# Performance work log

Measured on AMD Instinct MI355X. Metric: run time of the kernel, lower is better.

Reference implementation:

```python
import jax, jax.numpy as jnp
import numpy as np
from jax import lax

B, C_IN, H, W = 16, 2048, 16, 16
HIDDEN, N_ANC = 512, 9
N_POS, N_NEG = 2048, 2048
TOT = B * N_ANC * H * W  # 36864 = flat conf logits; also rows of reg.view(-1,4)


def _xyxy_to_cxcywh(b):
    x1, y1, x2, y2 = b[..., 0], b[..., 1], b[..., 2], b[..., 3]
    return jnp.stack([(x1 + x2) * 0.5, (y1 + y2) * 0.5, x2 - x1, y2 - y1], axis=-1)


def _cxcywh_to_xyxy(b):
    cx, cy, w, h = b[..., 0], b[..., 1], b[..., 2], b[..., 3]
    return jnp.stack([cx - w * 0.5, cy - h * 0.5, cx + w * 0.5, cy + h * 0.5], axis=-1)


def _rand_boxes(key, n):
    # valid xyxy boxes on the 16x16 feature-map coordinate grid, w,h in [1,4]
    k1, k2 = jax.random.split(key)
    xy = jax.random.uniform(k1, (n, 2), jnp.float32) * 12.0
    wh = 1.0 + jax.random.uniform(k2, (n, 2), jnp.float32) * 3.0
    return jnp.concatenate([xy, xy + wh], axis=-1)


def setup_inputs() -> dict:
    key = jax.random.key(0)
    ks = jax.random.split(key, 10)
    feature_map = jax.random.normal(ks[0], (B, C_IN, H, W), jnp.float32)
    pos_anc_ind = jax.random.randint(ks[1], (N_POS,), 0, TOT)
    neg_anc_ind = jax.random.randint(ks[2], (N_NEG,), 0, TOT)
    pos_anc_coords = _rand_boxes(ks[3], N_POS)
    gt_bboxes_pos = _rand_boxes(ks[4], N_POS)
    s1 = 1.0 / np.sqrt(C_IN * 9)
    W1 = jax.random.uniform(ks[5], (HIDDEN, C_IN, 3, 3), jnp.float32, -s1, s1)
    b1 = jnp.zeros((HIDDEN,), jnp.float32)
    s2 = 1.0 / np.sqrt(HIDDEN)
    Wc = jax.random.uniform(ks[6], (N_ANC, HIDDEN), jnp.float32, -s2, s2)
    bc = jnp.zeros((N_ANC,), jnp.float32)
    Wr = jax.random.uniform(ks[7], (N_ANC * 4, HIDDEN), jnp.float32, -s2, s2)
    br = jnp.zeros((N_ANC * 4,), jnp.float32)
    return {"feature_map": feature_map, "pos_anc_coords": pos_anc_coords,
            "gt_bboxes_pos": gt_bboxes_pos, "W1": W1, "b1": b1, "Wc": Wc,
            "bc": bc, "Wr": Wr, "br": br,
            "pos_anc_ind": pos_anc_ind, "neg_anc_ind": neg_anc_ind}


def generate_proposals(anchors, offsets):
    a = _xyxy_to_cxcywh(anchors)
    p = jnp.stack([a[:, 0] + offsets[:, 0] * a[:, 2],
                   a[:, 1] + offsets[:, 1] * a[:, 3],
                   a[:, 2] * jnp.exp(offsets[:, 2]),
                   a[:, 3] * jnp.exp(offsets[:, 3])], axis=-1)
    return _cxcywh_to_xyxy(p)


def calc_gt_offsets(anc, gt):
    a = _xyxy_to_cxcywh(anc)
    g = _xyxy_to_cxcywh(gt)
    tx = (g[:, 0] - a[:, 0]) / a[:, 2]
    ty = (g[:, 1] - a[:, 1]) / a[:, 3]
    tw = jnp.log(g[:, 2] / a[:, 2])
    th = jnp.log(g[:, 3] / a[:, 3])
    return jnp.stack([tx, ty, tw, th], axis=-1)


def reference(feature_map, pos_anc_coords, gt_bboxes_pos, W1, b1, Wc, bc, Wr, br,
              pos_anc_ind, neg_anc_ind):
    # ProposalModule: conv3x3 -> (dropout=identity in eval) -> relu -> 1x1 heads
    out = lax.conv_general_dilated(feature_map, W1, (1, 1), 'SAME',
                                   dimension_numbers=('NCHW', 'OIHW', 'NCHW'))
    out = jax.nn.relu(out + b1[None, :, None, None])
    conf = jnp.einsum('bchw,oc->bohw', out, Wc) + bc[None, :, None, None]   # [B,9,H,W]
    reg = jnp.einsum('bchw,oc->bohw', out, Wr) + br[None, :, None, None]    # [B,36,H,W]
    # irregular flat gathers, exactly mirroring torch .flatten()/.view(-1,4)
    conf_pos = conf.reshape(-1)[pos_anc_ind]
    conf_neg = conf.reshape(-1)[neg_anc_ind]
    offsets_pos = reg.reshape(-1, 4)[pos_anc_ind]
    proposals = generate_proposals(pos_anc_coords, offsets_pos)
    gt_offsets = calc_gt_offsets(pos_anc_coords, gt_bboxes_pos)
    # BCE-with-logits, targets 1 for pos / 0 for neg, reduction='sum' / B
    cls_loss = (jnp.sum(jax.nn.softplus(-conf_pos)) + jnp.sum(jax.nn.softplus(conf_neg))) / B
    # smooth L1 (beta=1), reduction='sum' / B
    d = offsets_pos - gt_offsets
    ad = jnp.abs(d)
    reg_loss = jnp.sum(jnp.where(ad < 1.0, 0.5 * d * d, ad - 0.5)) / B
    total_rpn_loss = 1.0 * cls_loss + 5.0 * reg_loss  # w_conf=1, w_reg=5
    return total_rpn_loss, proposals
```

## Files before the change

kernel.cpp:

```cpp
#include <hip/hip_runtime.h>
#include <hip/hip_bf16.h>
#include <stdint.h>

#define CIN 2048
#define HID 512
#define NPOS 2048
#define NNEG 2048

#define BM 256
#define BN 128
#define BK 64
#define NSPLIT 4
#define A_ELEMS (BM * BK)
#define B_ELEMS (BN * BK)

typedef __attribute__((ext_vector_type(8))) short s16x8;
typedef __attribute__((ext_vector_type(4))) short s16x4;
typedef __attribute__((ext_vector_type(4))) float f32x4;
typedef unsigned short ushort_t;

static __device__ __forceinline__ unsigned short f2bf(float f) {
    union { float f; unsigned int i; } v; v.f = f;
    unsigned int r = v.i + 0x7FFF + ((v.i >> 16) & 1);
    return (unsigned short)(r >> 16);
}

typedef __attribute__((address_space(1))) const void gvoid_t;
typedef __attribute__((address_space(3))) void lvoid_t;
static __device__ __forceinline__ void gload16(const void* g, void* l) {
    __builtin_amdgcn_global_load_lds((gvoid_t*)g, (lvoid_t*)l, 16, 0, 0);
}

__global__ __launch_bounds__(256) void k_prep(const float* __restrict__ F,
                                              const float* __restrict__ W1,
                                              ushort_t* __restrict__ Fp,
                                              ushort_t* __restrict__ Wt2) {
    __shared__ float tile[64][17];
    __shared__ float buf[512 * 9];
    int bid = blockIdx.x;
    int t = threadIdx.x;
    if (bid < 256) {
        int b = bid >> 4, y = bid & 15;
        for (int ic0 = 0; ic0 < CIN; ic0 += 64) {
            {
                int ci = t >> 2, xg = t & 3;
                const float4 v = *(const float4*)&F[((size_t)(b * CIN + ic0 + ci) * 16 + y) * 16 + xg * 4];
                tile[ci][xg * 4 + 0] = v.x;
                tile[ci][xg * 4 + 1] = v.y;
                tile[ci][xg * 4 + 2] = v.z;
                tile[ci][xg * 4 + 3] = v.w;
            }
            __syncthreads();
            {
                int x = t >> 4, cig = t & 15;
                s16x4 o;
#pragma unroll
                for (int j = 0; j < 4; ++j) o[j] = (short)f2bf(tile[cig * 4 + j][x]);
                *(s16x4*)&Fp[((size_t)(b * 18 + y + 1) * 18 + (x + 1)) * CIN + ic0 + cig * 4] = o;
            }
            __syncthreads();
        }
    } else if (bid < 768) {
        int oc = bid - 256;
        for (int ic0 = 0; ic0 < CIN; ic0 += 512) {
            const float* src = W1 + ((size_t)oc * CIN + ic0) * 9;
            for (int i = t; i < 512 * 9; i += 256) buf[i] = src[i];
            __syncthreads();
            for (int s = t; s < 9 * 64; s += 256) {
                int k = s >> 6, g = s & 63;
                s16x8 v;
#pragma unroll
                for (int j = 0; j < 8; ++j) v[j] = (short)f2bf(buf[(g * 8 + j) * 9 + k]);
                *(s16x8*)&Wt2[((size_t)(k * HID + oc)) * CIN + ic0 + g * 8] = v;
            }
            __syncthreads();
        }
    } else {
        const s16x8 z = {0, 0, 0, 0, 0, 0, 0, 0};
        for (int idx = (bid - 768) * 256 + t; idx < 16 * 68 * 256; idx += 64 * 256) {
            int seg = idx & 255;
            int cell = (idx >> 8) % 68;
            int b = idx / (68 * 256);
            int Y, X;
            if (cell < 18)      { Y = 0;         X = cell; }
            else if (cell < 36) { Y = 17;        X = cell - 18; }
            else if (cell < 52) { Y = cell - 35; X = 0; }
            else                { Y = cell - 51; X = 17; }
            *(s16x8*)&Fp[((size_t)(b * 18 + Y) * 18 + X) * CIN + seg * 8] = z;
        }
    }
}

__global__ __launch_bounds__(512, 2) void k_gemm(const ushort_t* __restrict__ Fp,
                                                 const ushort_t* __restrict__ Wt2,
                                                 float* __restrict__ Part) {
    extern __shared__ ushort_t ldsbuf[];
    ushort_t* As = ldsbuf;
    ushort_t* Bs = ldsbuf + 3 * A_ELEMS;

    int bid = blockIdx.x;
    int pair = bid & 15, rb = bid >> 4;
    int split = pair >> 2, cb = pair & 3;
    int icBase = split * (CIN / NSPLIT);
    int m0 = rb * BM, oc0 = cb * BN;
    int t = threadIdx.x;
    int wid = t >> 6, lane = t & 63;
    int wr = wid >> 1, wn = wid & 1;
    int hi = lane >> 4, lo = lane & 15;

    f32x4 acc[4][4];
#pragma unroll
    for (int a = 0; a < 4; ++a)
#pragma unroll
        for (int b = 0; b < 4; ++b) acc[a][b] = (f32x4){0.f, 0.f, 0.f, 0.f};

    int Abase[4], Bbase[2];
#pragma unroll
    for (int j = 0; j < 4; ++j) {
        int li = j * 512 + t;
        int row = li >> 3;
        int sg = (li & 7) ^ (row & 7);
        int m = m0 + row;
        int b = m >> 8, y = (m >> 4) & 15, x = m & 15;
        Abase[j] = ((b * 18 + y) * 18 + x) * CIN + sg * 8;
    }
#pragma unroll
    for (int j = 0; j < 2; ++j) {
        int li = j * 512 + t;
        int row = li >> 3;
        int sg = (li & 7) ^ (row & 7);
        Bbase[j] = (oc0 + row) * CIN + sg * 8;
    }
    int aidx[4][2], bidx[4][2];
#pragma unroll
    for (int fm = 0; fm < 4; ++fm)
#pragma unroll
        for (int ks = 0; ks < 2; ++ks) {
            int r = wr * 64 + fm * 16 + lo;
            aidx[fm][ks] = r * BK + ((ks * 32 + hi * 8) ^ ((r & 7) << 3));
            int rB = wn * 64 + fm * 16 + lo;
            bidx[fm][ks] = rB * BK + ((ks * 32 + hi * 8) ^ ((rB & 7) << 3));
        }

    const int nsteps = (CIN / NSPLIT / BK) * 9;

#define STAGE_A(BUF, S)                                                              \
    do {                                                                             \
        int kidx_ = (S) % 9, icc_ = (S) / 9;                                         \
        int ak_ = ((kidx_ / 3) * 18 + (kidx_ - 3 * (kidx_ / 3))) * CIN + icBase + icc_ * BK; \
        ushort_t* dA_ = As + (BUF) * A_ELEMS;                                        \
        _Pragma("unroll") for (int j_ = 0; j_ < 4; ++j_)                             \
            gload16(Fp + Abase[j_] + ak_, dA_ + (size_t)(j_ * 512 + t) * 8);         \
    } while (0)
#define STAGE_B(BUF, S)                                                              \
    do {                                                                             \
        int kidx_ = (S) % 9, icc_ = (S) / 9;                                         \
        int bk_ = kidx_ * HID * CIN + icBase + icc_ * BK;                            \
        ushort_t* dB_ = Bs + (BUF) * B_ELEMS;                                        \
        _Pragma("unroll") for (int j_ = 0; j_ < 2; ++j_)                             \
            gload16(Wt2 + Bbase[j_] + bk_, dB_ + (size_t)(j_ * 512 + t) * 8);        \
    } while (0)

    STAGE_A(0, 0); STAGE_B(0, 0);
    STAGE_A(1, 1); STAGE_B(1, 1);
    asm volatile("s_waitcnt vmcnt(6)" ::: "memory");
    __builtin_amdgcn_s_barrier();
    __builtin_amdgcn_sched_barrier(0);

    int bi = 0;
#pragma unroll 1
    for (int step = 0; step < nsteps; ++step) {
        const ushort_t* cA = As + bi * A_ELEMS;
        const ushort_t* cB = Bs + bi * B_ELEMS;
        int b2 = (bi >= 1) ? bi - 1 : 2;
        if (step + 2 < nsteps) { STAGE_A(b2, step + 2); STAGE_B(b2, step + 2); }
        s16x8 af[4][2], bf[4][2];
#pragma unroll
        for (int ks = 0; ks < 2; ++ks) {
#pragma unroll
            for (int fm = 0; fm < 4; ++fm) af[fm][ks] = *(const s16x8*)&cA[aidx[fm][ks]];
#pragma unroll
            for (int fn = 0; fn < 4; ++fn) bf[fn][ks] = *(const s16x8*)&cB[bidx[fn][ks]];
        }
        __builtin_amdgcn_s_setprio(1);
#pragma unroll
        for (int fm = 0; fm < 4; ++fm)
#pragma unroll
            for (int fn = 0; fn < 4; ++fn)
#pragma unroll
                for (int ks = 0; ks < 2; ++ks)
                    acc[fm][fn] = __builtin_amdgcn_mfma_f32_16x16x32_bf16(
                        af[fm][ks], bf[fn][ks], acc[fm][fn], 0, 0, 0);
        __builtin_amdgcn_s_setprio(0);
        if (step + 2 < nsteps) {
            asm volatile("s_waitcnt vmcnt(6)" ::: "memory");
            __builtin_amdgcn_s_barrier();
            __builtin_amdgcn_sched_barrier(0);
        } else if (step + 1 < nsteps) {
            asm volatile("s_waitcnt vmcnt(0)" ::: "memory");
            __builtin_amdgcn_s_barrier();
            __builtin_amdgcn_sched_barrier(0);
        }
        bi = (bi == 2) ? 0 : bi + 1;
    }
#undef STAGE_A
#undef STAGE_B

#pragma unroll
    for (int fm = 0; fm < 4; ++fm)
#pragma unroll
        for (int fn = 0; fn < 4; ++fn)
#pragma unroll
            for (int r = 0; r < 4; ++r) {
                int gm = m0 + wr * 64 + fm * 16 + hi * 4 + r;
                int gn = oc0 + wn * 64 + fn * 16 + lo;
                Part[((size_t)split * 4096 + gm) * HID + gn] = acc[fm][fn][r];
            }
}

__global__ __launch_bounds__(256) void k_heads(const float* __restrict__ Part,
                                               const float* __restrict__ b1,
                                               const float* __restrict__ Wc,
                                               const float* __restrict__ bc,
                                               const float* __restrict__ Wr,
                                               const float* __restrict__ br,
                                               float* __restrict__ conf,
                                               float* __restrict__ reg) {
    extern __shared__ ushort_t hsm[];
    ushort_t* Ah = hsm;
    ushort_t* Wh = hsm + 16 * HID;
    int t = threadIdx.x;
    int wid = t >> 6, lane = t & 63;
    int hi = lane >> 4, lo = lane & 15;
    int row0 = blockIdx.x * 16;

#pragma unroll
    for (int i = 0; i < 8; ++i) {
        int pos = i * 256 + t;
        int r = pos >> 7, c4 = (pos & 127) * 4;
        float4 s = {0.f, 0.f, 0.f, 0.f};
#pragma unroll
        for (int sp = 0; sp < NSPLIT; ++sp) {
            const float4 v = *(const float4*)&Part[((size_t)sp * 4096 + row0 + r) * HID + c4];
            s.x += v.x; s.y += v.y; s.z += v.z; s.w += v.w;
        }
        s.x = fmaxf(s.x + b1[c4 + 0], 0.f);
        s.y = fmaxf(s.y + b1[c4 + 1], 0.f);
        s.z = fmaxf(s.z + b1[c4 + 2], 0.f);
        s.w = fmaxf(s.w + b1[c4 + 3], 0.f);
        s16x4 o = {(short)f2bf(s.x), (short)f2bf(s.y), (short)f2bf(s.z), (short)f2bf(s.w)};
        int phys = r * HID + ((((c4 >> 3) ^ (r & 7)) << 3) | (c4 & 7));
        *(s16x4*)&Ah[phys] = o;
    }
#pragma unroll
    for (int i = 0; i < 12; ++i) {
        int sid = i * 256 + t;
        int o = sid >> 6, sg = sid & 63;
        s16x8 v;
#pragma unroll
        for (int j = 0; j < 8; ++j) {
            float w = 0.f;
            if (o < 9) w = Wc[o * HID + sg * 8 + j];
            else if (o < 45) w = Wr[(size_t)(o - 9) * HID + sg * 8 + j];
            v[j] = (short)f2bf(w);
        }
        *(s16x8*)&Wh[o * HID + ((sg ^ (o & 7)) << 3)] = v;
    }
    __syncthreads();
    if (wid != 0) return;

    f32x4 acc[3];
#pragma unroll
    for (int fn = 0; fn < 3; ++fn) acc[fn] = (f32x4){0.f, 0.f, 0.f, 0.f};
#pragma unroll 1
    for (int kf = 0; kf < 16; ++kf) {
        int rA = lo;
        s16x8 a_ = *(const s16x8*)&Ah[rA * HID + ((kf * 32 + hi * 8) ^ ((rA & 7) << 3))];
#pragma unroll
        for (int fn = 0; fn < 3; ++fn) {
            int rB = fn * 16 + lo;
            s16x8 b_ = *(const s16x8*)&Wh[rB * HID + ((kf * 32 + hi * 8) ^ ((rB & 7) << 3))];
            acc[fn] = __builtin_amdgcn_mfma_f32_16x16x32_bf16(a_, b_, acc[fn], 0, 0, 0);
        }
    }
#pragma unroll
    for (int fn = 0; fn < 3; ++fn)
#pragma unroll
        for (int r = 0; r < 4; ++r) {
            int gm = row0 + hi * 4 + r;
            int o = fn * 16 + lo;
            float v = acc[fn][r];
            if (o < 9) conf[gm * 9 + o] = v + bc[o];
            else if (o < 45) reg[gm * 36 + (o - 9)] = v + br[o - 9];
        }
}

static __device__ __forceinline__ float softplus(float x) {
    return log1pf(expf(-fabsf(x))) + fmaxf(x, 0.f);
}

__global__ __launch_bounds__(1024) void k_loss(const float* __restrict__ conf,
                                               const float* __restrict__ reg,
                                               const int* __restrict__ pos_ind,
                                               const int* __restrict__ neg_ind,
                                               const float* __restrict__ anc,
                                               const float* __restrict__ gt,
                                               float* __restrict__ out) {
    int t = threadIdx.x;
    float cls = 0.f, rloss = 0.f;
    for (int p = t; p < NPOS; p += 1024) {
        int ind = pos_ind[p];
        {
            int b = ind / 2304, r = ind % 2304;
            int c = r >> 8, r2 = r & 255;
            float cv = conf[(b * 256 + r2) * 9 + c];
            cls += softplus(-cv);
        }
        float off[4];
#pragma unroll
        for (int j = 0; j < 4; ++j) {
            int e = 4 * ind + j;
            int b = e / 9216, r = e % 9216;
            int c = r >> 8, r2 = r & 255;
            off[j] = reg[(b * 256 + r2) * 36 + c];
        }
        float ax1 = anc[4 * p], ay1 = anc[4 * p + 1], ax2 = anc[4 * p + 2], ay2 = anc[4 * p + 3];
        float acx = (ax1 + ax2) * 0.5f, acy = (ay1 + ay2) * 0.5f;
        float aw = ax2 - ax1, ah = ay2 - ay1;
        float pcx = acx + off[0] * aw, pcy = acy + off[1] * ah;
        float pw = aw * expf(off[2]), ph = ah * expf(off[3]);
        out[1 + 4 * p + 0] = pcx - pw * 0.5f;
        out[1 + 4 * p + 1] = pcy - ph * 0.5f;
        out[1 + 4 * p + 2] = pcx + pw * 0.5f;
        out[1 + 4 * p + 3] = pcy + ph * 0.5f;
        float gx1 = gt[4 * p], gy1 = gt[4 * p + 1], gx2 = gt[4 * p + 2], gy2 = gt[4 * p + 3];
        float gcx = (gx1 + gx2) * 0.5f, gcy = (gy1 + gy2) * 0.5f;
        float gw = gx2 - gx1, gh = gy2 - gy1;
        float tv[4];
        tv[0] = (gcx - acx) / aw;
        tv[1] = (gcy - acy) / ah;
        tv[2] = logf(gw / aw);
        tv[3] = logf(gh / ah);
#pragma unroll
        for (int j = 0; j < 4; ++j) {
            float d = off[j] - tv[j];
            float ad = fabsf(d);
            rloss += (ad < 1.f) ? 0.5f * d * d : ad - 0.5f;
        }
    }
    for (int q = t; q < NNEG; q += 1024) {
        int ind = neg_ind[q];
        int b = ind / 2304, r = ind % 2304;
        int c = r >> 8, r2 = r & 255;
        float cv = conf[(b * 256 + r2) * 9 + c];
        cls += softplus(cv);
    }
    __shared__ float s1[1024], s2[1024];
    s1[t] = cls;
    s2[t] = rloss;
    __syncthreads();
    for (int s = 512; s > 0; s >>= 1) {
        if (t < s) {
            s1[t] += s1[t + s];
            s2[t] += s2[t + s];
        }
        __syncthreads();
    }
    if (t == 0) out[0] = (s1[0] + 5.f * s2[0]) / 16.f;
}

extern "C" void kernel_launch(void* const* d_in, const int* in_sizes, int n_in,
                              void* d_out, int out_size, void* d_ws, size_t ws_size,
                              hipStream_t stream) {
    const float* F   = (const float*)d_in[0];
    const float* anc = (const float*)d_in[1];
    const float* gt  = (const float*)d_in[2];
    const float* W1  = (const float*)d_in[3];
    const float* b1  = (const float*)d_in[4];
    const float* Wc  = (const float*)d_in[5];
    const float* bc  = (const float*)d_in[6];
    const float* Wr  = (const float*)d_in[7];
    const float* br  = (const float*)d_in[8];
    const int* pos_ind = (const int*)d_in[9];
    const int* neg_ind = (const int*)d_in[10];
    float* out = (float*)d_out;

    char* ws = (char*)d_ws;
    const size_t FP_BYTES   = (size_t)16 * 18 * 18 * CIN * 2;
    const size_t WT_BYTES   = (size_t)9 * HID * CIN * 2;
    const size_t PART_ONE   = (size_t)4096 * HID * 4;
    const size_t CONF_BYTES = (size_t)4096 * 9 * 4;

    ushort_t* Fp  = (ushort_t*)ws;
    ushort_t* Wt2 = (ushort_t*)(ws + FP_BYTES);
    float* Part   = (float*)(ws + FP_BYTES + WT_BYTES);
    float* conf   = (float*)(ws + FP_BYTES + WT_BYTES + (size_t)NSPLIT * PART_ONE);
    float* reg    = (float*)(ws + FP_BYTES + WT_BYTES + (size_t)NSPLIT * PART_ONE + CONF_BYTES);

    const int GEMM_LDS = 3 * (A_ELEMS + B_ELEMS) * 2;
    hipFuncSetAttribute((const void*)k_gemm, hipFuncAttributeMaxDynamicSharedMemorySize, GEMM_LDS);
    const int HEADS_LDS = (16 + 48) * HID * 2;
    hipFuncSetAttribute((const void*)k_heads, hipFuncAttributeMaxDynamicSharedMemorySize, HEADS_LDS);

    k_prep<<<832, 256, 0, stream>>>(F, W1, Fp, Wt2);
    k_gemm<<<(4096 / BM) * (HID / BN) * NSPLIT, 512, GEMM_LDS, stream>>>(Fp, Wt2, Part);
    k_heads<<<256, 256, HEADS_LDS, stream>>>(Part, b1, Wc, bc, Wr, br, conf, reg);
    k_loss<<<1, 1024, 0, stream>>>(conf, reg, pos_ind, neg_ind, anc, gt, out);
}
```

Before: 130.8 us.

## Enlarge GEMM tile to 256x256, double-buffer LDS, raise split-K to eight

The conv GEMM tile grows from 256x128 to 256x256, so each wave computes a 128x64 sub-tile, which raises operand reuse per LDS load. The LDS pipeline drops from triple to double buffering and waits vmcnt(0) every step, because the larger tile leaves no room for three stages. Split-K goes from 4 to 8 when the workspace allows, which keeps the grid at 256 blocks but doubles the partial-sum traffic read by the heads kernel. Larger accumulators raise register pressure, and the shallower pipeline exposes more load latency.

```diff
diff --git a/kernel.cpp b/kernel.cpp
--- a/kernel.cpp
+++ b/kernel.cpp
@@ -8,9 +8,8 @@
 #define NNEG 2048
 
 #define BM 256
-#define BN 128
+#define BN 256
 #define BK 64
-#define NSPLIT 4
 #define A_ELEMS (BM * BK)
 #define B_ELEMS (BN * BK)
 
@@ -93,28 +92,30 @@
 
 __global__ __launch_bounds__(512, 2) void k_gemm(const ushort_t* __restrict__ Fp,
                                                  const ushort_t* __restrict__ Wt2,
-                                                 float* __restrict__ Part) {
+                                                 float* __restrict__ Part,
+                                                 int icLen, int nPairs) {
     extern __shared__ ushort_t ldsbuf[];
     ushort_t* As = ldsbuf;
-    ushort_t* Bs = ldsbuf + 3 * A_ELEMS;
+    ushort_t* Bs = ldsbuf + 2 * A_ELEMS;
 
     int bid = blockIdx.x;
-    int pair = bid & 15, rb = bid >> 4;
-    int split = pair >> 2, cb = pair & 3;
-    int icBase = split * (CIN / NSPLIT);
+    int rb = bid / nPairs;
+    int pair = bid - rb * nPairs;
+    int split = pair >> 1, cb = pair & 1;
+    int icBase = split * icLen;
     int m0 = rb * BM, oc0 = cb * BN;
     int t = threadIdx.x;
     int wid = t >> 6, lane = t & 63;
-    int wr = wid >> 1, wn = wid & 1;
+    int wr = wid >> 2, wn = wid & 3;
     int hi = lane >> 4, lo = lane & 15;
 
-    f32x4 acc[4][4];
-#pragma unroll
-    for (int a = 0; a < 4; ++a)
+    f32x4 acc[8][4];
+#pragma unroll
+    for (int a = 0; a < 8; ++a)
 #pragma unroll
         for (int b = 0; b < 4; ++b) acc[a][b] = (f32x4){0.f, 0.f, 0.f, 0.f};
 
-    int Abase[4], Bbase[2];
+    int Abase[4], Bbase[4];
 #pragma unroll
     for (int j = 0; j < 4; ++j) {
         int li = j * 512 + t;
@@ -123,68 +124,61 @@
         int m = m0 + row;
         int b = m >> 8, y = (m >> 4) & 15, x = m & 15;
         Abase[j] = ((b * 18 + y) * 18 + x) * CIN + sg * 8;
-    }
-#pragma unroll
-    for (int j = 0; j < 2; ++j) {
-        int li = j * 512 + t;
-        int row = li >> 3;
-        int sg = (li & 7) ^ (row & 7);
         Bbase[j] = (oc0 + row) * CIN + sg * 8;
     }
-    int aidx[4][2], bidx[4][2];
-#pragma unroll
-    for (int fm = 0; fm < 4; ++fm)
+    int aidx[8][2], bidx[4][2];
+#pragma unroll
+    for (int fm = 0; fm < 8; ++fm)
 #pragma unroll
         for (int ks = 0; ks < 2; ++ks) {
-            int r = wr * 64 + fm * 16 + lo;
+            int r = wr * 128 + fm * 16 + lo;
             aidx[fm][ks] = r * BK + ((ks * 32 + hi * 8) ^ ((r & 7) << 3));
-            int rB = wn * 64 + fm * 16 + lo;
-            bidx[fm][ks] = rB * BK + ((ks * 32 + hi * 8) ^ ((rB & 7) << 3));
-        }
-
-    const int nsteps = (CIN / NSPLIT / BK) * 9;
-
-#define STAGE_A(BUF, S)                                                              \
+        }
+#pragma unroll
+    for (int fn = 0; fn < 4; ++fn)
+#pragma unroll
+        for (int ks = 0; ks < 2; ++ks) {
+            int rB = wn * 64 + fn * 16 + lo;
+            bidx[fn][ks] = rB * BK + ((ks * 32 + hi * 8) ^ ((rB & 7) << 3));
+        }
+
+    const int nsteps = (icLen / BK) * 9;
+
+#define STAGE(BUF, S)                                                                \
     do {                                                                             \
         int kidx_ = (S) % 9, icc_ = (S) / 9;                                         \
         int ak_ = ((kidx_ / 3) * 18 + (kidx_ - 3 * (kidx_ / 3))) * CIN + icBase + icc_ * BK; \
+        int bk_ = kidx_ * HID * CIN + icBase + icc_ * BK;                            \
         ushort_t* dA_ = As + (BUF) * A_ELEMS;                                        \
-        _Pragma("unroll") for (int j_ = 0; j_ < 4; ++j_)                             \
+        ushort_t* dB_ = Bs + (BUF) * B_ELEMS;                                        \
+        _Pragma("unroll") for (int j_ = 0; j_ < 4; ++j_) {                           \
             gload16(Fp + Abase[j_] + ak_, dA_ + (size_t)(j_ * 512 + t) * 8);         \
+            gload16(Wt2 + Bbase[j_] + bk_, dB_ + (size_t)(j_ * 512 + t) * 8);        \
+        }                                                                            \
     } while (0)
-#define STAGE_B(BUF, S)                                                              \
-    do {                                                                             \
-        int kidx_ = (S) % 9, icc_ = (S) / 9;                                         \
-        int bk_ = kidx_ * HID * CIN + icBase + icc_ * BK;                            \
-        ushort_t* dB_ = Bs + (BUF) * B_ELEMS;                                        \
-        _Pragma("unroll") for (int j_ = 0; j_ < 2; ++j_)                             \
-            gload16(Wt2 + Bbase[j_] + bk_, dB_ + (size_t)(j_ * 512 + t) * 8);        \
-    } while (0)
-
-    STAGE_A(0, 0); STAGE_B(0, 0);
-    STAGE_A(1, 1); STAGE_B(1, 1);
-    asm volatile("s_waitcnt vmcnt(6)" ::: "memory");
+
+    STAGE(0, 0);
+    asm volatile("s_waitcnt vmcnt(0)" ::: "memory");
     __builtin_amdgcn_s_barrier();
     __builtin_amdgcn_sched_barrier(0);
 
-    int bi = 0;
+    int cur = 0;
 #pragma unroll 1
     for (int step = 0; step < nsteps; ++step) {
-        const ushort_t* cA = As + bi * A_ELEMS;
-        const ushort_t* cB = Bs + bi * B_ELEMS;
-        int b2 = (bi >= 1) ? bi - 1 : 2;
-        if (step + 2 < nsteps) { STAGE_A(b2, step + 2); STAGE_B(b2, step + 2); }
-        s16x8 af[4][2], bf[4][2];
+        const ushort_t* cA = As + cur * A_ELEMS;
+        const ushort_t* cB = Bs + cur * B_ELEMS;
+        if (step + 1 < nsteps) STAGE(cur ^ 1, step + 1);
+        s16x8 af[8][2], bf[4][2];
 #pragma unroll
         for (int ks = 0; ks < 2; ++ks) {
 #pragma unroll
-            for (int fm = 0; fm < 4; ++fm) af[fm][ks] = *(const s16x8*)&cA[aidx[fm][ks]];
+            for (int fm = 0; fm < 8; ++fm) af[fm][ks] = *(const s16x8*)&cA[aidx[fm][ks]];
 #pragma unroll
             for (int fn = 0; fn < 4; ++fn) bf[fn][ks] = *(const s16x8*)&cB[bidx[fn][ks]];
         }
         __builtin_amdgcn_s_setprio(1);
 #pragma unroll
-        for (int fm = 0; fm < 4; ++fm)
+        for (int fm = 0; fm < 8; ++fm)
 #pragma unroll
             for (int fn = 0; fn < 4; ++fn)
 #pragma unroll
@@ -192,33 +186,28 @@
                     acc[fm][fn] = __builtin_amdgcn_mfma_f32_16x16x32_bf16(
                         af[fm][ks], bf[fn][ks], acc[fm][fn], 0, 0, 0);
         __builtin_amdgcn_s_setprio(0);
-        if (step + 2 < nsteps) {
-            asm volatile("s_waitcnt vmcnt(6)" ::: "memory");
-            __builtin_amdgcn_s_barrier();
-            __builtin_amdgcn_sched_barrier(0);
-        } else if (step + 1 < nsteps) {
+        if (step + 1 < nsteps) {
             asm volatile("s_waitcnt vmcnt(0)" ::: "memory");
             __builtin_amdgcn_s_barrier();
             __builtin_amdgcn_sched_barrier(0);
         }
-        bi = (bi == 2) ? 0 : bi + 1;
-    }
-#undef STAGE_A
-#undef STAGE_B
-
-#pragma unroll
-    for (int fm = 0; fm < 4; ++fm)
+        cur ^= 1;
+    }
+#undef STAGE
+
+#pragma unroll
+    for (int fm = 0; fm < 8; ++fm)
 #pragma unroll
         for (int fn = 0; fn < 4; ++fn)
 #pragma unroll
             for (int r = 0; r < 4; ++r) {
-                int gm = m0 + wr * 64 + fm * 16 + hi * 4 + r;
+                int gm = m0 + wr * 128 + fm * 16 + hi * 4 + r;
                 int gn = oc0 + wn * 64 + fn * 16 + lo;
                 Part[((size_t)split * 4096 + gm) * HID + gn] = acc[fm][fn][r];
             }
 }
 
-__global__ __launch_bounds__(256) void k_heads(const float* __restrict__ Part,
+__global__ __launch_bounds__(256) void k_heads(const float* __restrict__ Part, int ns,
                                                const float* __restrict__ b1,
                                                const float* __restrict__ Wc,
                                                const float* __restrict__ bc,
@@ -239,8 +228,7 @@
         int pos = i * 256 + t;
         int r = pos >> 7, c4 = (pos & 127) * 4;
         float4 s = {0.f, 0.f, 0.f, 0.f};
-#pragma unroll
-        for (int sp = 0; sp < NSPLIT; ++sp) {
+        for (int sp = 0; sp < ns; ++sp) {
             const float4 v = *(const float4*)&Part[((size_t)sp * 4096 + row0 + r) * HID + c4];
             s.x += v.x; s.y += v.y; s.z += v.z; s.w += v.w;
         }
@@ -390,20 +378,27 @@
     const size_t WT_BYTES   = (size_t)9 * HID * CIN * 2;
     const size_t PART_ONE   = (size_t)4096 * HID * 4;
     const size_t CONF_BYTES = (size_t)4096 * 9 * 4;
+    const size_t REG_BYTES  = (size_t)4096 * 36 * 4;
+
+    int NS = 8;
+    while (NS > 1 &&
+           FP_BYTES + WT_BYTES + (size_t)NS * PART_ONE + CONF_BYTES + REG_BYTES > ws_size)
+        NS >>= 1;
+    int icLen = CIN / NS;
 
     ushort_t* Fp  = (ushort_t*)ws;
     ushort_t* Wt2 = (ushort_t*)(ws + FP_BYTES);
     float* Part   = (float*)(ws + FP_BYTES + WT_BYTES);
-    float* conf   = (float*)(ws + FP_BYTES + WT_BYTES + (size_t)NSPLIT * PART_ONE);
-    float* reg    = (float*)(ws + FP_BYTES + WT_BYTES + (size_t)NSPLIT * PART_ONE + CONF_BYTES);
-
-    const int GEMM_LDS = 3 * (A_ELEMS + B_ELEMS) * 2;
+    float* conf   = (float*)(ws + FP_BYTES + WT_BYTES + (size_t)NS * PART_ONE);
+    float* reg    = (float*)(ws + FP_BYTES + WT_BYTES + (size_t)NS * PART_ONE + CONF_BYTES);
+
+    const int GEMM_LDS = 2 * (A_ELEMS + B_ELEMS) * 2;
     hipFuncSetAttribute((const void*)k_gemm, hipFuncAttributeMaxDynamicSharedMemorySize, GEMM_LDS);
     const int HEADS_LDS = (16 + 48) * HID * 2;
     hipFuncSetAttribute((const void*)k_heads, hipFuncAttributeMaxDynamicSharedMemorySize, HEADS_LDS);
 
     k_prep<<<832, 256, 0, stream>>>(F, W1, Fp, Wt2);
-    k_gemm<<<(4096 / BM) * (HID / BN) * NSPLIT, 512, GEMM_LDS, stream>>>(Fp, Wt2, Part);
-    k_heads<<<256, 256, HEADS_LDS, stream>>>(Part, b1, Wc, bc, Wr, br, conf, reg);
+    k_gemm<<<(4096 / BM) * (HID / BN) * NS, 512, GEMM_LDS, stream>>>(Fp, Wt2, Part, icLen, 2 * NS);
+    k_heads<<<256, 256, HEADS_LDS, stream>>>(Part, NS, b1, Wc, bc, Wr, br, conf, reg);
     k_loss<<<1, 1024, 0, stream>>>(conf, reg, pos_ind, neg_ind, anc, gt, out);
 }
```

Result: slower. 138.6 us (+6.0%).
